# Performance work log

Measured on AMD Instinct MI355X. Metric: run time of the kernel, lower is better.

The kernel has to match this reference:

```python
import jax, jax.numpy as jnp
import numpy as np

D_MODEL = 1024
N_HEADS = 16
D_HEAD = D_MODEL // N_HEADS
WIN = 128        # local_window
HALF = WIN // 2  # 64
KW = 2 * WIN     # kv window length per block (half-left + block + half-right)


def setup_inputs() -> dict:
    key = jax.random.key(0)
    ks = jax.random.split(key, 6)
    B, L = 2, 8192
    s = 0.02
    return {
        "x": jax.random.normal(ks[0], (B, L, D_MODEL), dtype=jnp.float32),
        "wq": jax.random.normal(ks[1], (D_MODEL, D_MODEL), dtype=jnp.float32) * s,
        "wk": jax.random.normal(ks[2], (D_MODEL, D_MODEL), dtype=jnp.float32) * s,
        "wv": jax.random.normal(ks[3], (D_MODEL, D_MODEL), dtype=jnp.float32) * s,
        "wo": jax.random.normal(ks[4], (D_MODEL, D_MODEL), dtype=jnp.float32) * s,
        "bo": jax.random.normal(ks[5], (D_MODEL,), dtype=jnp.float32) * s,
    }


def _rotate_half(t):
    t1, t2 = jnp.split(t, 2, axis=-1)
    return jnp.concatenate([-t2, t1], axis=-1)


def _rope(L, dtype):
    inv_freq = 1.0 / (10000.0 ** (jnp.arange(0, D_HEAD, 2, dtype=jnp.float32) / D_HEAD))
    t = jnp.arange(L, dtype=jnp.float32)
    freqs = t[:, None] * inv_freq[None, :]          # [L, D_HEAD/2]
    emb = jnp.concatenate([freqs, freqs], axis=-1)  # [L, D_HEAD]
    return jnp.cos(emb).astype(dtype), jnp.sin(emb).astype(dtype)


def reference(x, wq, wk, wv, wo, bo):
    B, L, D = x.shape
    H, Dh = N_HEADS, D_HEAD
    # projections (torch Linear: x @ W.T)
    q = (x @ wq.T).reshape(B, L, H, Dh).transpose(0, 2, 1, 3)  # [B,H,L,Dh]
    k = (x @ wk.T).reshape(B, L, H, Dh).transpose(0, 2, 1, 3)
    v = (x @ wv.T).reshape(B, L, H, Dh).transpose(0, 2, 1, 3)
    cos, sin = _rope(L, x.dtype)                    # [L, Dh]
    q = q * cos + _rotate_half(q) * sin
    k = k * cos + _rotate_half(k) * sin
    nb = L // WIN
    starts = jnp.arange(nb) * WIN - HALF            # window start per block
    idx = starts[:, None] + jnp.arange(KW)          # [nb, KW] kv indices
    valid = (idx >= 0) & (idx < L)
    idxc = jnp.clip(idx, 0, L - 1)
    kw = k[:, :, idxc]                              # [B,H,nb,KW,Dh]
    vw = v[:, :, idxc]
    qb = q.reshape(B, H, nb, WIN, Dh)
    scores = jnp.einsum('bhnqd,bhnkd->bhnqk', qb, kw) / np.sqrt(Dh).astype(x.dtype)
    scores = jnp.where(valid[None, None, :, None, :], scores, -jnp.inf)
    attn = jax.nn.softmax(scores, axis=-1)
    out = jnp.einsum('bhnqk,bhnkd->bhnqd', attn, vw).reshape(B, H, L, Dh)
    out = out.transpose(0, 2, 1, 3).reshape(B, L, D)
    return out @ wo.T + bo
```

## Files before the change

### kernel.cpp

```cpp
#include <hip/hip_runtime.h>
#include <cstdint>
#include <math.h>

#define L_SEQ 8192
#define DM    1024
#define NQK   2048

typedef unsigned short u16;
typedef __bf16 bf16;
typedef bf16  bf16x8 __attribute__((ext_vector_type(8)));
typedef float f32x4  __attribute__((ext_vector_type(4)));

__device__ __forceinline__ u16 f2bf(float f) {
    unsigned u = __float_as_uint(f);
    u += 0x7fffu + ((u >> 16) & 1u);
    return (u16)(u >> 16);
}

__device__ __forceinline__ f32x4 mfma16(bf16x8 a, bf16x8 b, f32x4 c) {
    return __builtin_amdgcn_mfma_f32_16x16x32_bf16(a, b, c, 0, 0, 0);
}

__device__ __forceinline__ void gld_lds16(const u16* g, u16* l) {
    __builtin_amdgcn_global_load_lds((const __attribute__((address_space(1))) void*)g,
                                     (__attribute__((address_space(3))) void*)l,
                                     16, 0, 0);
}

__global__ void cvt_bf16(const float* __restrict__ src, u16* __restrict__ dst, int n8) {
    int i = blockIdx.x * 256 + threadIdx.x;
    if (i >= n8) return;
    const float4* s4 = (const float4*)src;
    float4 a = s4[2 * i], b = s4[2 * i + 1];
    union { uint4 u; u16 h[8]; } r;
    r.h[0] = f2bf(a.x); r.h[1] = f2bf(a.y); r.h[2] = f2bf(a.z); r.h[3] = f2bf(a.w);
    r.h[4] = f2bf(b.x); r.h[5] = f2bf(b.y); r.h[6] = f2bf(b.z); r.h[7] = f2bf(b.w);
    ((uint4*)dst)[i] = r.u;
}

__global__ void rope_tbl(float2* __restrict__ t) {
    int idx = blockIdx.x * 256 + threadIdx.x;
    int pos = idx >> 5, i = idx & 31;
    float invf = exp2f(-0.4152410118609191f * (float)i);
    float s, c;
    sincosf((float)pos * invf, &s, &c);
    t[idx] = make_float2(c, s);
}

__global__ __launch_bounds__(256) void gemm_qkv_fused(
    const u16* __restrict__ X,
    const u16* __restrict__ W,
    const float2* __restrict__ rope,
    u16* __restrict__ Y,
    u16* __restrict__ Vt)
{
    __shared__ __align__(16) char smem[34816];
    u16* As = (u16*)smem;
    u16* Bs = As + 128 * 64;

    const int n0 = blockIdx.x * 128;
    const int m0 = blockIdx.y * 128;
    const int tid = threadIdx.x;
    const int lane = tid & 63, wid = tid >> 6;
    const int wm = wid >> 1, wn = wid & 1;
    const int quad = lane >> 4, ln = lane & 15;

    const f32x4 fz = {0.f, 0.f, 0.f, 0.f};
    f32x4 acc[4][4];
    for (int a = 0; a < 4; a++)
        for (int b = 0; b < 4; b++) acc[a][b] = fz;

    for (int k0 = 0; k0 < DM; k0 += 64) {
        __syncthreads();
        #pragma unroll
        for (int i = 0; i < 4; ++i) {
            int idx = i * 256 + tid;
            int row = idx >> 3, cl = idx & 7;
            int cg = cl ^ (row & 7);
            gld_lds16(X + (size_t)(m0 + row) * DM + k0 + cg * 8, As + idx * 8);
            gld_lds16(W + (size_t)(n0 + row) * DM + k0 + cg * 8, Bs + idx * 8);
        }
        __syncthreads();
        #pragma unroll
        for (int ks = 0; ks < 2; ks++) {
            bf16x8 af[4], bfr[4];
            #pragma unroll
            for (int t = 0; t < 4; t++) {
                int ra = wm * 64 + t * 16 + ln;
                af[t]  = *(const bf16x8*)(As + ra * 64 + (((ks * 4 + quad) ^ (ln & 7)) * 8));
                int rb = wn * 64 + t * 16 + ln;
                bfr[t] = *(const bf16x8*)(Bs + rb * 64 + (((ks * 4 + quad) ^ (ln & 7)) * 8));
            }
            #pragma unroll
            for (int mt = 0; mt < 4; mt++)
                #pragma unroll
                for (int nt = 0; nt < 4; nt++)
                    acc[mt][nt] = mfma16(af[mt], bfr[nt], acc[mt][nt]);
        }
    }
    __syncthreads();

    if (n0 < 2048) {
        #pragma unroll
        for (int mt = 0; mt < 4; mt++)
            #pragma unroll
            for (int reg = 0; reg < 4; reg++) {
                int rg = (m0 + wm * 64 + mt * 16 + quad * 4 + reg) & (L_SEQ - 1);
                const float2* rp = rope + rg * 32;
                #pragma unroll
                for (int nt = 0; nt < 2; nt++) {
                    float2 cs = rp[nt * 16 + ln];
                    float x1 = acc[mt][nt][reg], x2 = acc[mt][nt + 2][reg];
                    acc[mt][nt][reg]     = x1 * cs.x - x2 * cs.y;
                    acc[mt][nt + 2][reg] = x2 * cs.x + x1 * cs.y;
                }
            }
        u16* Es = (u16*)smem;
        #pragma unroll
        for (int mt = 0; mt < 4; mt++)
            #pragma unroll
            for (int nt = 0; nt < 4; nt++)
                #pragma unroll
                for (int reg = 0; reg < 4; reg++) {
                    int rl = wm * 64 + mt * 16 + quad * 4 + reg;
                    int cl = wn * 64 + nt * 16 + ln;
                    Es[rl * 136 + cl] = f2bf(acc[mt][nt][reg]);
                }
        __syncthreads();
        #pragma unroll
        for (int i = 0; i < 8; i++) {
            int idx = i * 256 + tid;
            int row = idx >> 4, ch = (idx & 15) * 8;
            uint4 v = *(const uint4*)(Es + row * 136 + ch);
            *(uint4*)(Y + (size_t)(m0 + row) * NQK + n0 + ch) = v;
        }
    } else {
        u16* Es = (u16*)smem;
        #pragma unroll
        for (int mt = 0; mt < 4; mt++)
            #pragma unroll
            for (int nt = 0; nt < 4; nt++)
                #pragma unroll
                for (int reg = 0; reg < 4; reg++) {
                    int rl = wm * 64 + mt * 16 + quad * 4 + reg;
                    int cl = wn * 64 + nt * 16 + ln;
                    Es[cl * 136 + rl] = f2bf(acc[mt][nt][reg]);
                }
        __syncthreads();
        const int bb = m0 >> 13, seq0 = m0 & (L_SEQ - 1);
        #pragma unroll
        for (int i = 0; i < 8; i++) {
            int idx = i * 256 + tid;
            int dr = idx >> 4, ch = (idx & 15) * 8;
            uint4 v = *(const uint4*)(Es + dr * 136 + ch);
            int gc = n0 - 2048 + dr;
            *(uint4*)(Vt + (size_t)(bb * 1024 + gc) * L_SEQ + seq0 + ch) = v;
        }
    }
}

__global__ __launch_bounds__(256) void gemm_oproj(
    const u16* __restrict__ A,
    const u16* __restrict__ Wo,
    const float* __restrict__ bias,
    float* __restrict__ Out)
{
    __shared__ __align__(16) char smem[34816];
    u16* As = (u16*)smem;
    u16* Bs = As + 128 * 64;

    const int n0 = blockIdx.x * 128;
    const int m0 = blockIdx.y * 128;
    const int tid = threadIdx.x;
    const int lane = tid & 63, wid = tid >> 6;
    const int wm = wid >> 1, wn = wid & 1;
    const int quad = lane >> 4, ln = lane & 15;

    const f32x4 fz = {0.f, 0.f, 0.f, 0.f};
    f32x4 acc[4][4];
    for (int a = 0; a < 4; a++)
        for (int b = 0; b < 4; b++) acc[a][b] = fz;

    for (int k0 = 0; k0 < DM; k0 += 64) {
        __syncthreads();
        #pragma unroll
        for (int i = 0; i < 4; ++i) {
            int idx = i * 256 + tid;
            int row = idx >> 3, cl = idx & 7;
            int cg = cl ^ (row & 7);
            gld_lds16(A  + (size_t)(m0 + row) * DM + k0 + cg * 8, As + idx * 8);
            gld_lds16(Wo + (size_t)(n0 + row) * DM + k0 + cg * 8, Bs + idx * 8);
        }
        __syncthreads();
        #pragma unroll
        for (int ks = 0; ks < 2; ks++) {
            bf16x8 af[4], bfr[4];
            #pragma unroll
            for (int t = 0; t < 4; t++) {
                int ra = wm * 64 + t * 16 + ln;
                af[t]  = *(const bf16x8*)(As + ra * 64 + (((ks * 4 + quad) ^ (ln & 7)) * 8));
                int rb = wn * 64 + t * 16 + ln;
                bfr[t] = *(const bf16x8*)(Bs + rb * 64 + (((ks * 4 + quad) ^ (ln & 7)) * 8));
            }
            #pragma unroll
            for (int mt = 0; mt < 4; mt++)
                #pragma unroll
                for (int nt = 0; nt < 4; nt++)
                    acc[mt][nt] = mfma16(af[mt], bfr[nt], acc[mt][nt]);
        }
    }

    float* Ef = (float*)smem;
    for (int hh = 0; hh < 2; ++hh) {
        __syncthreads();
        if (wm == hh) {
            #pragma unroll
            for (int mt = 0; mt < 4; mt++)
                #pragma unroll
                for (int nt = 0; nt < 4; nt++)
                    #pragma unroll
                    for (int reg = 0; reg < 4; reg++) {
                        int rl = mt * 16 + quad * 4 + reg;
                        int cl = wn * 64 + nt * 16 + ln;
                        Ef[rl * 136 + cl] = acc[mt][nt][reg] + bias[n0 + cl];
                    }
        }
        __syncthreads();
        #pragma unroll
        for (int i = 0; i < 8; i++) {
            int idx = i * 256 + tid;
            int row = idx >> 5, ch = (idx & 31) * 4;
            float4 v = *(const float4*)(Ef + row * 136 + ch);
            *(float4*)(Out + (size_t)(m0 + hh * 64 + row) * DM + n0 + ch) = v;
        }
    }
}

__global__ __launch_bounds__(512, 4) void attn(
    const u16* __restrict__ QK,
    const u16* __restrict__ Vt,
    u16* __restrict__ AO)
{
    __shared__ __align__(16) u16 Ks[256 * 64];
    __shared__ __align__(16) u16 Vs[64 * 256];
    __shared__ __align__(16) u16 pbuf[8][512];

    const int blk = blockIdx.x;
    const int h   = blockIdx.y;
    const int b   = blockIdx.z;
    const int tid = threadIdx.x;
    const int lane = tid & 63, w = tid >> 6;
    const int quad = lane >> 4, ln = lane & 15;
    const int wstart = blk * 128 - 64;
    const size_t bbase = (size_t)b * L_SEQ;

    const u16* Kg = QK + 1024 + h * 64;
    const u16* Vg = Vt + (size_t)(b * 1024 + h * 64) * L_SEQ;

    #pragma unroll
    for (int i = 0; i < 4; i++) {
        int c = i * 512 + tid;
        int row = c >> 3, cl = c & 7, cg = cl ^ (row & 7);
        int kr = wstart + row;
        kr = kr < 0 ? 0 : (kr > L_SEQ - 1 ? L_SEQ - 1 : kr);
        gld_lds16(Kg + (size_t)(bbase + kr) * NQK + cg * 8, Ks + c * 8);
    }
    #pragma unroll
    for (int i = 0; i < 4; i++) {
        int c = i * 512 + tid;
        int d = c >> 5, kc = c & 31, cg = kc ^ (d & 7);
        int key = wstart + cg * 8;
        key = key < 0 ? 0 : (key > L_SEQ - 8 ? L_SEQ - 8 : key);
        gld_lds16(Vg + (size_t)d * L_SEQ + key, Vs + c * 8);
    }

    const int qrow = blk * 128 + w * 16 + ln;
    const u16* qp = QK + (bbase + qrow) * NQK + h * 64 + quad * 8;
    bf16x8 aq0 = *(const bf16x8*)qp;
    bf16x8 aq1 = *(const bf16x8*)(qp + 32);
    __syncthreads();

    const f32x4 fz = {0.f, 0.f, 0.f, 0.f};
    f32x4 s[16];
    #pragma unroll
    for (int nt = 0; nt < 16; nt++) {
        int row = nt * 16 + ln;
        bf16x8 b0 = *(const bf16x8*)(Ks + row * 64 + ((quad       ^ (ln & 7)) * 8));
        bf16x8 b1 = *(const bf16x8*)(Ks + row * 64 + (((4 + quad) ^ (ln & 7)) * 8));
        f32x4 t = mfma16(aq0, b0, fz);
        t = mfma16(aq1, b1, t);
        s[nt] = t;
    }
    __syncthreads();

    const float SC = 0.125f * 1.4426950408889634f;
    float mr[4] = {-INFINITY, -INFINITY, -INFINITY, -INFINITY};
    #pragma unroll
    for (int nt = 0; nt < 16; nt++) {
        int key = wstart + nt * 16 + ln;
        bool valid = (key >= 0) && (key < L_SEQ);
        #pragma unroll
        for (int r = 0; r < 4; r++) {
            float v = valid ? s[nt][r] * SC : -INFINITY;
            s[nt][r] = v;
            mr[r] = fmaxf(mr[r], v);
        }
    }
    #pragma unroll
    for (int off = 1; off < 16; off <<= 1)
        #pragma unroll
        for (int r = 0; r < 4; r++) mr[r] = fmaxf(mr[r], __shfl_xor(mr[r], off));

    float lr[4] = {0.f, 0.f, 0.f, 0.f};
    #pragma unroll
    for (int nt = 0; nt < 16; nt++)
        #pragma unroll
        for (int r = 0; r < 4; r++) {
            float p = exp2f(s[nt][r] - mr[r]);
            s[nt][r] = p;
            lr[r] += p;
        }
    #pragma unroll
    for (int off = 1; off < 16; off <<= 1)
        #pragma unroll
        for (int r = 0; r < 4; r++) lr[r] += __shfl_xor(lr[r], off);
    float rl[4];
    #pragma unroll
    for (int r = 0; r < 4; r++) rl[r] = 1.f / lr[r];

    u16* pb = pbuf[w];
    f32x4 o[4] = {fz, fz, fz, fz};
    #pragma unroll
    for (int ks = 0; ks < 8; ks++) {
        #pragma unroll
        for (int n2 = 0; n2 < 2; n2++) {
            int nt = ks * 2 + n2;
            #pragma unroll
            for (int r = 0; r < 4; r++)
                pb[(quad * 4 + r) * 32 + ((n2 * 16 + ln) ^ (quad * 8))] = f2bf(s[nt][r]);
        }
        bf16x8 ap = *(const bf16x8*)(pb + ln * 32 + ((quad * 8) ^ (((ln >> 2) & 3) * 8)));
        #pragma unroll
        for (int dt = 0; dt < 4; dt++) {
            int d = dt * 16 + ln;
            bf16x8 vb = *(const bf16x8*)(Vs + d * 256 + (((ks * 4 + quad) ^ (ln & 7)) * 8));
            o[dt] = mfma16(ap, vb, o[dt]);
        }
    }

    u16* AOs = Ks;
    #pragma unroll
    for (int dt = 0; dt < 4; dt++)
        #pragma unroll
        for (int r = 0; r < 4; r++)
            AOs[(w * 16 + quad * 4 + r) * 72 + dt * 16 + ln] = f2bf(o[dt][r] * rl[r]);
    __syncthreads();
    #pragma unroll
    for (int i = 0; i < 2; i++) {
        int c = i * 512 + tid;
        int row = c >> 3, ch = (c & 7) * 8;
        uint4 v = *(const uint4*)(AOs + row * 72 + ch);
        *(uint4*)(AO + (bbase + blk * 128 + row) * DM + h * 64 + ch) = v;
    }
}

extern "C" void kernel_launch(void* const* d_in, const int* in_sizes, int n_in,
                              void* d_out, int out_size, void* d_ws, size_t ws_size,
                              hipStream_t stream) {
    const float* x  = (const float*)d_in[0];
    const float* wq = (const float*)d_in[1];
    const float* wk = (const float*)d_in[2];
    const float* wv = (const float*)d_in[3];
    const float* wo = (const float*)d_in[4];
    const float* bo = (const float*)d_in[5];
    float* out = (float*)d_out;

    char* ws = (char*)d_ws;
    const size_t MB = 1024 * 1024;
    u16*   xb  = (u16*)ws;
    u16*   fqk = (u16*)(ws + 32 * MB);
    u16*   vt  = (u16*)(ws + 96 * MB);
    u16*   wf  = (u16*)(ws + 128 * MB);
    float2* rt = (float2*)(ws + 134 * MB);
    u16*   wob = (u16*)(ws + 136 * MB);
    u16*   aob = xb;

    cvt_bf16<<<8192, 256, 0, stream>>>(x, xb, 2097152);
    cvt_bf16<<<512, 256, 0, stream>>>(wq, wf, 131072);
    cvt_bf16<<<512, 256, 0, stream>>>(wk, wf + 1024 * 1024, 131072);
    cvt_bf16<<<512, 256, 0, stream>>>(wv, wf + 2 * 1024 * 1024, 131072);
    cvt_bf16<<<512, 256, 0, stream>>>(wo, wob, 131072);
    rope_tbl<<<1024, 256, 0, stream>>>(rt);

    gemm_qkv_fused<<<dim3(24, 128), 256, 0, stream>>>(xb, wf, rt, fqk, vt);
    attn<<<dim3(64, 16, 2), 512, 0, stream>>>(fqk, vt, aob);
    gemm_oproj<<<dim3(8, 128), 256, 0, stream>>>(aob, wob, bo, out);
}
```

Measured before the change: 376.2 us.

## Rewrite QKV and output GEMMs as 256x256 double-buffered pipelined 8-wave kernels

Both projection GEMMs move from 128x128 tiles with 4 waves and a synchronous load-then-compute loop to 256x256 tiles with 8 waves. The new loop double-buffers LDS and issues the next tiles' global-to-LDS loads between MFMA phases, using explicit vmcnt waits, barriers and setprio. Block IDs are remapped to group neighbouring tiles for L2 reuse, and the epilogues are split into halves or quarters to fit the LDS staging buffer. This aims to hide memory latency and raise MFMA utilisation, at the cost of 128KB LDS per block, more registers and fewer blocks in the grid.

```diff
diff --git a/kernel.cpp b/kernel.cpp
--- a/kernel.cpp
+++ b/kernel.cpp
@@ -26,6 +26,14 @@
                                      (__attribute__((address_space(3))) void*)l,
                                      16, 0, 0);
 }
+
+__device__ __forceinline__ void bar() {
+    __builtin_amdgcn_sched_barrier(0);
+    __builtin_amdgcn_s_barrier();
+    __builtin_amdgcn_sched_barrier(0);
+}
+#define VMCNT4() asm volatile("s_waitcnt vmcnt(4)" ::: "memory")
+#define VMCNT0() asm volatile("s_waitcnt vmcnt(0)" ::: "memory")
 
 __global__ void cvt_bf16(const float* __restrict__ src, u16* __restrict__ dst, int n8) {
     int i = blockIdx.x * 256 + threadIdx.x;
@@ -47,65 +55,155 @@
     t[idx] = make_float2(c, s);
 }
 
-__global__ __launch_bounds__(256) void gemm_qkv_fused(
+
+#define STAGE_A(kt, ha, par) do { \
+    gld_lds16(baseA + (size_t)(ha) * 131072 + (size_t)(kt) * 64, \
+              ldsA + (par) * 16384 + (ha) * 8192); \
+    gld_lds16(baseA + (size_t)(ha) * 131072 + 65536 + (size_t)(kt) * 64, \
+              ldsA + (par) * 16384 + (ha) * 8192 + 4096); \
+} while (0)
+#define STAGE_B(kt, hb, par) do { \
+    gld_lds16(baseB + (size_t)(hb) * 131072 + (size_t)(kt) * 64, \
+              ldsB + (par) * 16384 + (hb) * 8192); \
+    gld_lds16(baseB + (size_t)(hb) * 131072 + 65536 + (size_t)(kt) * 64, \
+              ldsB + (par) * 16384 + (hb) * 8192 + 4096); \
+} while (0)
+
+__global__ __launch_bounds__(512, 2) void gemm_qkv_fused(
     const u16* __restrict__ X,
     const u16* __restrict__ W,
     const float2* __restrict__ rope,
     u16* __restrict__ Y,
     u16* __restrict__ Vt)
 {
-    __shared__ __align__(16) char smem[34816];
-    u16* As = (u16*)smem;
-    u16* Bs = As + 128 * 64;
-
-    const int n0 = blockIdx.x * 128;
-    const int m0 = blockIdx.y * 128;
+    __shared__ __align__(16) u16 smem[65536];
+    u16* SA = smem;
+    u16* SB = smem + 32768;
+
+    int id = (int)blockIdx.x;
+    id = (id & 7) * 96 + (id >> 3);
+    const int n0 = (id % 12) * 256;
+    const int m0 = (id / 12) * 256;
+
     const int tid = threadIdx.x;
-    const int lane = tid & 63, wid = tid >> 6;
-    const int wm = wid >> 1, wn = wid & 1;
+    const int lane = tid & 63, w = tid >> 6;
+    const int wm = w >> 2, wn = w & 3;
     const int quad = lane >> 4, ln = lane & 15;
 
+    const int r0 = tid >> 3;
+    const int cgs = (tid & 7) ^ (r0 & 7);
+    const u16* baseA = X + (size_t)(m0 + r0) * DM + cgs * 8;
+    const u16* baseB = W + (size_t)(n0 + r0) * DM + cgs * 8;
+    u16* ldsA = SA + tid * 8;
+    u16* ldsB = SB + tid * 8;
+
+    const int c0 = (quad ^ (ln & 7)) * 8;
+    const int c1 = ((quad + 4) ^ (ln & 7)) * 8;
+    const int aoff = wm * 8192 + ln * 64;
+    const int boff = (wn >> 1) * 8192 + ((wn & 1) * 64 + ln) * 64;
+
     const f32x4 fz = {0.f, 0.f, 0.f, 0.f};
-    f32x4 acc[4][4];
-    for (int a = 0; a < 4; a++)
+    f32x4 acc[8][4];
+    #pragma unroll
+    for (int a = 0; a < 8; a++)
+        #pragma unroll
         for (int b = 0; b < 4; b++) acc[a][b] = fz;
 
-    for (int k0 = 0; k0 < DM; k0 += 64) {
-        __syncthreads();
-        #pragma unroll
-        for (int i = 0; i < 4; ++i) {
-            int idx = i * 256 + tid;
-            int row = idx >> 3, cl = idx & 7;
-            int cg = cl ^ (row & 7);
-            gld_lds16(X + (size_t)(m0 + row) * DM + k0 + cg * 8, As + idx * 8);
-            gld_lds16(W + (size_t)(n0 + row) * DM + k0 + cg * 8, Bs + idx * 8);
-        }
-        __syncthreads();
-        #pragma unroll
-        for (int ks = 0; ks < 2; ks++) {
-            bf16x8 af[4], bfr[4];
-            #pragma unroll
-            for (int t = 0; t < 4; t++) {
-                int ra = wm * 64 + t * 16 + ln;
-                af[t]  = *(const bf16x8*)(As + ra * 64 + (((ks * 4 + quad) ^ (ln & 7)) * 8));
-                int rb = wn * 64 + t * 16 + ln;
-                bfr[t] = *(const bf16x8*)(Bs + rb * 64 + (((ks * 4 + quad) ^ (ln & 7)) * 8));
-            }
-            #pragma unroll
-            for (int mt = 0; mt < 4; mt++)
-                #pragma unroll
-                for (int nt = 0; nt < 4; nt++)
-                    acc[mt][nt] = mfma16(af[mt], bfr[nt], acc[mt][nt]);
-        }
-    }
-    __syncthreads();
+    STAGE_A(0, 0, 0); STAGE_A(0, 1, 0);
+    STAGE_B(0, 0, 0); STAGE_B(0, 1, 0);
+    STAGE_B(1, 0, 1); STAGE_B(1, 1, 1);
+    VMCNT4();
+    bar();
+
+    #pragma unroll 2
+    for (int u = 0; u < 16; ++u) {
+        const int par = u & 1;
+        const u16* pa = SA + par * 16384 + aoff;
+        const u16* pb = SB + par * 16384 + boff;
+        bf16x8 af[4][2], bf[4][2];
+
+        #pragma unroll
+        for (int m = 0; m < 4; m++) {
+            af[m][0] = *(const bf16x8*)(pa + m * 1024 + c0);
+            af[m][1] = *(const bf16x8*)(pa + m * 1024 + c1);
+        }
+        #pragma unroll
+        for (int n = 0; n < 2; n++) {
+            bf[n][0] = *(const bf16x8*)(pb + n * 1024 + c0);
+            bf[n][1] = *(const bf16x8*)(pb + n * 1024 + c1);
+        }
+        STAGE_A((u + 1) & 15, 0, par ^ 1);
+        bar();
+        __builtin_amdgcn_s_setprio(1);
+        #pragma unroll
+        for (int m = 0; m < 4; m++)
+            #pragma unroll
+            for (int n = 0; n < 2; n++) {
+                acc[m][n] = mfma16(af[m][0], bf[n][0], acc[m][n]);
+                acc[m][n] = mfma16(af[m][1], bf[n][1], acc[m][n]);
+            }
+        __builtin_amdgcn_s_setprio(0);
+        bar();
+
+        #pragma unroll
+        for (int n = 0; n < 2; n++) {
+            bf[2 + n][0] = *(const bf16x8*)(pb + (2 + n) * 1024 + c0);
+            bf[2 + n][1] = *(const bf16x8*)(pb + (2 + n) * 1024 + c1);
+        }
+        STAGE_A((u + 1) & 15, 1, par ^ 1);
+        bar();
+        __builtin_amdgcn_s_setprio(1);
+        #pragma unroll
+        for (int m = 0; m < 4; m++)
+            #pragma unroll
+            for (int n = 0; n < 2; n++) {
+                acc[m][2 + n] = mfma16(af[m][0], bf[2 + n][0], acc[m][2 + n]);
+                acc[m][2 + n] = mfma16(af[m][1], bf[2 + n][1], acc[m][2 + n]);
+            }
+        __builtin_amdgcn_s_setprio(0);
+        bar();
+
+        #pragma unroll
+        for (int m = 0; m < 4; m++) {
+            af[m][0] = *(const bf16x8*)(pa + (4 + m) * 1024 + c0);
+            af[m][1] = *(const bf16x8*)(pa + (4 + m) * 1024 + c1);
+        }
+        STAGE_B((u + 2) & 15, 0, par);
+        bar();
+        __builtin_amdgcn_s_setprio(1);
+        #pragma unroll
+        for (int m = 0; m < 4; m++)
+            #pragma unroll
+            for (int n = 0; n < 2; n++) {
+                acc[4 + m][2 + n] = mfma16(af[m][0], bf[2 + n][0], acc[4 + m][2 + n]);
+                acc[4 + m][2 + n] = mfma16(af[m][1], bf[2 + n][1], acc[4 + m][2 + n]);
+            }
+        __builtin_amdgcn_s_setprio(0);
+        bar();
+
+        STAGE_B((u + 2) & 15, 1, par);
+        VMCNT4();
+        bar();
+        __builtin_amdgcn_s_setprio(1);
+        #pragma unroll
+        for (int m = 0; m < 4; m++)
+            #pragma unroll
+            for (int n = 0; n < 2; n++) {
+                acc[4 + m][n] = mfma16(af[m][0], bf[n][0], acc[4 + m][n]);
+                acc[4 + m][n] = mfma16(af[m][1], bf[n][1], acc[4 + m][n]);
+            }
+        __builtin_amdgcn_s_setprio(0);
+        bar();
+    }
+    VMCNT0();
+    bar();
 
     if (n0 < 2048) {
         #pragma unroll
-        for (int mt = 0; mt < 4; mt++)
+        for (int mt = 0; mt < 8; mt++)
             #pragma unroll
             for (int reg = 0; reg < 4; reg++) {
-                int rg = (m0 + wm * 64 + mt * 16 + quad * 4 + reg) & (L_SEQ - 1);
+                int rg = (m0 + wm * 128 + mt * 16 + quad * 4 + reg) & (L_SEQ - 1);
                 const float2* rp = rope + rg * 32;
                 #pragma unroll
                 for (int nt = 0; nt < 2; nt++) {
@@ -115,123 +213,211 @@
                     acc[mt][nt + 2][reg] = x2 * cs.x + x1 * cs.y;
                 }
             }
-        u16* Es = (u16*)smem;
-        #pragma unroll
-        for (int mt = 0; mt < 4; mt++)
-            #pragma unroll
-            for (int nt = 0; nt < 4; nt++)
+        u16* Es = smem;
+        #pragma unroll
+        for (int mh = 0; mh < 2; mh++) {
+            if (mh) __syncthreads();
+            if (wm == mh) {
                 #pragma unroll
-                for (int reg = 0; reg < 4; reg++) {
-                    int rl = wm * 64 + mt * 16 + quad * 4 + reg;
-                    int cl = wn * 64 + nt * 16 + ln;
-                    Es[rl * 136 + cl] = f2bf(acc[mt][nt][reg]);
-                }
-        __syncthreads();
-        #pragma unroll
-        for (int i = 0; i < 8; i++) {
-            int idx = i * 256 + tid;
-            int row = idx >> 4, ch = (idx & 15) * 8;
-            uint4 v = *(const uint4*)(Es + row * 136 + ch);
-            *(uint4*)(Y + (size_t)(m0 + row) * NQK + n0 + ch) = v;
+                for (int mt = 0; mt < 8; mt++)
+                    #pragma unroll
+                    for (int nt = 0; nt < 4; nt++)
+                        #pragma unroll
+                        for (int reg = 0; reg < 4; reg++)
+                            Es[(mt * 16 + quad * 4 + reg) * 264 + wn * 64 + nt * 16 + ln] =
+                                f2bf(acc[mt][nt][reg]);
+            }
+            __syncthreads();
+            #pragma unroll
+            for (int i = 0; i < 8; i++) {
+                int idx = i * 512 + tid;
+                int row = idx >> 5, ch = (idx & 31) * 8;
+                uint4 v = *(const uint4*)(Es + row * 264 + ch);
+                *(uint4*)(Y + (size_t)(m0 + mh * 128 + row) * NQK + n0 + ch) = v;
+            }
         }
     } else {
-        u16* Es = (u16*)smem;
-        #pragma unroll
-        for (int mt = 0; mt < 4; mt++)
-            #pragma unroll
-            for (int nt = 0; nt < 4; nt++)
+        u16* Es = smem;
+        const int bb = m0 >> 13, seq0 = m0 & (L_SEQ - 1);
+        #pragma unroll
+        for (int nh = 0; nh < 2; nh++) {
+            if (nh) __syncthreads();
+            if ((wn >> 1) == nh) {
                 #pragma unroll
-                for (int reg = 0; reg < 4; reg++) {
-                    int rl = wm * 64 + mt * 16 + quad * 4 + reg;
-                    int cl = wn * 64 + nt * 16 + ln;
-                    Es[cl * 136 + rl] = f2bf(acc[mt][nt][reg]);
-                }
-        __syncthreads();
-        const int bb = m0 >> 13, seq0 = m0 & (L_SEQ - 1);
-        #pragma unroll
-        for (int i = 0; i < 8; i++) {
-            int idx = i * 256 + tid;
-            int dr = idx >> 4, ch = (idx & 15) * 8;
-            uint4 v = *(const uint4*)(Es + dr * 136 + ch);
-            int gc = n0 - 2048 + dr;
-            *(uint4*)(Vt + (size_t)(bb * 1024 + gc) * L_SEQ + seq0 + ch) = v;
-        }
-    }
-}
-
-__global__ __launch_bounds__(256) void gemm_oproj(
+                for (int mt = 0; mt < 8; mt++)
+                    #pragma unroll
+                    for (int nt = 0; nt < 4; nt++)
+                        #pragma unroll
+                        for (int reg = 0; reg < 4; reg++)
+                            Es[((wn & 1) * 64 + nt * 16 + ln) * 264 + wm * 128 + mt * 16 + quad * 4 + reg] =
+                                f2bf(acc[mt][nt][reg]);
+            }
+            __syncthreads();
+            #pragma unroll
+            for (int i = 0; i < 8; i++) {
+                int idx = i * 512 + tid;
+                int dr = idx >> 5, ch = (idx & 31) * 8;
+                int gc = n0 - 2048 + nh * 128 + dr;
+                uint4 v = *(const uint4*)(Es + dr * 264 + ch);
+                *(uint4*)(Vt + (size_t)(bb * 1024 + gc) * L_SEQ + seq0 + ch) = v;
+            }
+        }
+    }
+}
+
+__global__ __launch_bounds__(512, 2) void gemm_oproj(
     const u16* __restrict__ A,
     const u16* __restrict__ Wo,
     const float* __restrict__ bias,
     float* __restrict__ Out)
 {
-    __shared__ __align__(16) char smem[34816];
-    u16* As = (u16*)smem;
-    u16* Bs = As + 128 * 64;
-
-    const int n0 = blockIdx.x * 128;
-    const int m0 = blockIdx.y * 128;
+    __shared__ __align__(16) u16 smem[65536];
+    u16* SA = smem;
+    u16* SB = smem + 32768;
+
+    int id = (int)blockIdx.x;
+    id = (id & 7) * 32 + (id >> 3);
+    const int n0 = (id & 3) * 256;
+    const int m0 = (id >> 2) * 256;
+
     const int tid = threadIdx.x;
-    const int lane = tid & 63, wid = tid >> 6;
-    const int wm = wid >> 1, wn = wid & 1;
+    const int lane = tid & 63, w = tid >> 6;
+    const int wm = w >> 2, wn = w & 3;
     const int quad = lane >> 4, ln = lane & 15;
 
+    const int r0 = tid >> 3;
+    const int cgs = (tid & 7) ^ (r0 & 7);
+    const u16* baseA = A  + (size_t)(m0 + r0) * DM + cgs * 8;
+    const u16* baseB = Wo + (size_t)(n0 + r0) * DM + cgs * 8;
+    u16* ldsA = SA + tid * 8;
+    u16* ldsB = SB + tid * 8;
+
+    const int c0 = (quad ^ (ln & 7)) * 8;
+    const int c1 = ((quad + 4) ^ (ln & 7)) * 8;
+    const int aoff = wm * 8192 + ln * 64;
+    const int boff = (wn >> 1) * 8192 + ((wn & 1) * 64 + ln) * 64;
+
     const f32x4 fz = {0.f, 0.f, 0.f, 0.f};
-    f32x4 acc[4][4];
-    for (int a = 0; a < 4; a++)
+    f32x4 acc[8][4];
+    #pragma unroll
+    for (int a = 0; a < 8; a++)
+        #pragma unroll
         for (int b = 0; b < 4; b++) acc[a][b] = fz;
 
-    for (int k0 = 0; k0 < DM; k0 += 64) {
-        __syncthreads();
-        #pragma unroll
-        for (int i = 0; i < 4; ++i) {
-            int idx = i * 256 + tid;
-            int row = idx >> 3, cl = idx & 7;
-            int cg = cl ^ (row & 7);
-            gld_lds16(A  + (size_t)(m0 + row) * DM + k0 + cg * 8, As + idx * 8);
-            gld_lds16(Wo + (size_t)(n0 + row) * DM + k0 + cg * 8, Bs + idx * 8);
-        }
-        __syncthreads();
-        #pragma unroll
-        for (int ks = 0; ks < 2; ks++) {
-            bf16x8 af[4], bfr[4];
-            #pragma unroll
-            for (int t = 0; t < 4; t++) {
-                int ra = wm * 64 + t * 16 + ln;
-                af[t]  = *(const bf16x8*)(As + ra * 64 + (((ks * 4 + quad) ^ (ln & 7)) * 8));
-                int rb = wn * 64 + t * 16 + ln;
-                bfr[t] = *(const bf16x8*)(Bs + rb * 64 + (((ks * 4 + quad) ^ (ln & 7)) * 8));
-            }
-            #pragma unroll
-            for (int mt = 0; mt < 4; mt++)
-                #pragma unroll
-                for (int nt = 0; nt < 4; nt++)
-                    acc[mt][nt] = mfma16(af[mt], bfr[nt], acc[mt][nt]);
-        }
-    }
+    STAGE_A(0, 0, 0); STAGE_A(0, 1, 0);
+    STAGE_B(0, 0, 0); STAGE_B(0, 1, 0);
+    STAGE_B(1, 0, 1); STAGE_B(1, 1, 1);
+    VMCNT4();
+    bar();
+
+    #pragma unroll 2
+    for (int u = 0; u < 16; ++u) {
+        const int par = u & 1;
+        const u16* pa = SA + par * 16384 + aoff;
+        const u16* pb = SB + par * 16384 + boff;
+        bf16x8 af[4][2], bf[4][2];
+
+        #pragma unroll
+        for (int m = 0; m < 4; m++) {
+            af[m][0] = *(const bf16x8*)(pa + m * 1024 + c0);
+            af[m][1] = *(const bf16x8*)(pa + m * 1024 + c1);
+        }
+        #pragma unroll
+        for (int n = 0; n < 2; n++) {
+            bf[n][0] = *(const bf16x8*)(pb + n * 1024 + c0);
+            bf[n][1] = *(const bf16x8*)(pb + n * 1024 + c1);
+        }
+        STAGE_A((u + 1) & 15, 0, par ^ 1);
+        bar();
+        __builtin_amdgcn_s_setprio(1);
+        #pragma unroll
+        for (int m = 0; m < 4; m++)
+            #pragma unroll
+            for (int n = 0; n < 2; n++) {
+                acc[m][n] = mfma16(af[m][0], bf[n][0], acc[m][n]);
+                acc[m][n] = mfma16(af[m][1], bf[n][1], acc[m][n]);
+            }
+        __builtin_amdgcn_s_setprio(0);
+        bar();
+
+        #pragma unroll
+        for (int n = 0; n < 2; n++) {
+            bf[2 + n][0] = *(const bf16x8*)(pb + (2 + n) * 1024 + c0);
+            bf[2 + n][1] = *(const bf16x8*)(pb + (2 + n) * 1024 + c1);
+        }
+        STAGE_A((u + 1) & 15, 1, par ^ 1);
+        bar();
+        __builtin_amdgcn_s_setprio(1);
+        #pragma unroll
+        for (int m = 0; m < 4; m++)
+            #pragma unroll
+            for (int n = 0; n < 2; n++) {
+                acc[m][2 + n] = mfma16(af[m][0], bf[2 + n][0], acc[m][2 + n]);
+                acc[m][2 + n] = mfma16(af[m][1], bf[2 + n][1], acc[m][2 + n]);
+            }
+        __builtin_amdgcn_s_setprio(0);
+        bar();
+
+        #pragma unroll
+        for (int m = 0; m < 4; m++) {
+            af[m][0] = *(const bf16x8*)(pa + (4 + m) * 1024 + c0);
+            af[m][1] = *(const bf16x8*)(pa + (4 + m) * 1024 + c1);
+        }
+        STAGE_B((u + 2) & 15, 0, par);
+        bar();
+        __builtin_amdgcn_s_setprio(1);
+        #pragma unroll
+        for (int m = 0; m < 4; m++)
+            #pragma unroll
+            for (int n = 0; n < 2; n++) {
+                acc[4 + m][2 + n] = mfma16(af[m][0], bf[2 + n][0], acc[4 + m][2 + n]);
+                acc[4 + m][2 + n] = mfma16(af[m][1], bf[2 + n][1], acc[4 + m][2 + n]);
+            }
+        __builtin_amdgcn_s_setprio(0);
+        bar();
+
+        STAGE_B((u + 2) & 15, 1, par);
+        VMCNT4();
+        bar();
+        __builtin_amdgcn_s_setprio(1);
+        #pragma unroll
+        for (int m = 0; m < 4; m++)
+            #pragma unroll
+            for (int n = 0; n < 2; n++) {
+                acc[4 + m][n] = mfma16(af[m][0], bf[n][0], acc[4 + m][n]);
+                acc[4 + m][n] = mfma16(af[m][1], bf[n][1], acc[4 + m][n]);
+            }
+        __builtin_amdgcn_s_setprio(0);
+        bar();
+    }
+    VMCNT0();
+    bar();
+
+    float b4[4];
+    #pragma unroll
+    for (int nt = 0; nt < 4; nt++) b4[nt] = bias[n0 + wn * 64 + nt * 16 + ln];
 
     float* Ef = (float*)smem;
-    for (int hh = 0; hh < 2; ++hh) {
-        __syncthreads();
-        if (wm == hh) {
+    #pragma unroll
+    for (int mq = 0; mq < 4; mq++) {
+        if (mq) __syncthreads();
+        if (wm == (mq >> 1)) {
             #pragma unroll
             for (int mt = 0; mt < 4; mt++)
                 #pragma unroll
                 for (int nt = 0; nt < 4; nt++)
                     #pragma unroll
-                    for (int reg = 0; reg < 4; reg++) {
-                        int rl = mt * 16 + quad * 4 + reg;
-                        int cl = wn * 64 + nt * 16 + ln;
-                        Ef[rl * 136 + cl] = acc[mt][nt][reg] + bias[n0 + cl];
-                    }
+                    for (int reg = 0; reg < 4; reg++)
+                        Ef[(mt * 16 + quad * 4 + reg) * 260 + wn * 64 + nt * 16 + ln] =
+                            acc[(mq & 1) * 4 + mt][nt][reg] + b4[nt];
         }
         __syncthreads();
         #pragma unroll
         for (int i = 0; i < 8; i++) {
-            int idx = i * 256 + tid;
-            int row = idx >> 5, ch = (idx & 31) * 4;
-            float4 v = *(const float4*)(Ef + row * 136 + ch);
-            *(float4*)(Out + (size_t)(m0 + hh * 64 + row) * DM + n0 + ch) = v;
+            int idx = i * 512 + tid;
+            int row = idx >> 6, ch = (idx & 63) * 4;
+            float4 v = *(const float4*)(Ef + row * 260 + ch);
+            *(float4*)(Out + (size_t)(m0 + mq * 64 + row) * DM + n0 + ch) = v;
         }
     }
 }
@@ -392,7 +578,7 @@
     cvt_bf16<<<512, 256, 0, stream>>>(wo, wob, 131072);
     rope_tbl<<<1024, 256, 0, stream>>>(rt);
 
-    gemm_qkv_fused<<<dim3(24, 128), 256, 0, stream>>>(xb, wf, rt, fqk, vt);
+    gemm_qkv_fused<<<768, 512, 0, stream>>>(xb, wf, rt, fqk, vt);
     attn<<<dim3(64, 16, 2), 512, 0, stream>>>(fqk, vt, aob);
-    gemm_oproj<<<dim3(8, 128), 256, 0, stream>>>(aob, wob, bo, out);
-}
+    gemm_oproj<<<256, 512, 0, stream>>>(aob, wob, bo, out);
+}
```

Measured after the change: 362.9 us. 1.04x faster.
